# Optimization experiments

Measured on AMD Instinct MI355X. Metric: run time of the kernel, lower is better.

Reference implementation:

```python
import jax, jax.numpy as jnp
import numpy as np

K = 3
PAD = 1


def bilinear_gather(xr, py, px):
    # xr: [B, G, H, W, C] channels-last per offset group; py/px: [B, G, H, W] sample coords
    B, G, H, W, C = xr.shape
    y0 = jnp.floor(py)
    x0 = jnp.floor(px)
    wy = py - y0
    wx = px - x0
    y0i = y0.astype(jnp.int32)
    x0i = x0.astype(jnp.int32)
    bi = jnp.arange(B)[:, None, None, None]
    gi = jnp.arange(G)[None, :, None, None]
    out = jnp.zeros(py.shape + (C,), xr.dtype)
    corners = (
        (0, 0, (1 - wy) * (1 - wx)),
        (0, 1, (1 - wy) * wx),
        (1, 0, wy * (1 - wx)),
        (1, 1, wy * wx),
    )
    for dy_, dx_, w in corners:
        yy = y0i + dy_
        xx = x0i + dx_
        valid = ((yy >= 0) & (yy < H) & (xx >= 0) & (xx < W)).astype(xr.dtype)
        yc = jnp.clip(yy, 0, H - 1)
        xc = jnp.clip(xx, 0, W - 1)
        v = xr[bi, gi, yc, xc]  # [B,G,H,W,C]
        out = out + (w * valid)[..., None] * v
    return out


def setup_inputs() -> dict:
    key = jax.random.key(0)
    k1, k2, k3, k4, k5 = jax.random.split(key, 5)
    B, Cin, H, W = 4, 64, 256, 256
    G, OC = 8, 64
    KK = K * K
    x = jax.random.normal(k1, (B, Cin, H, W), jnp.float32)
    offset = jax.random.normal(k2, (B, 2, G * KK, H, W), jnp.float32)
    mask = jax.random.normal(k3, (B, G * KK, H, W), jnp.float32)
    weight = jax.random.normal(k4, (OC, Cin // G, K, K), jnp.float32) * 0.05
    bias = jax.random.normal(k5, (OC,), jnp.float32) * 0.01
    return {"x": x, "offset": offset, "mask": mask, "weight": weight, "bias": bias}


def reference(x, offset, mask, weight, bias):
    B, Cin, H, W = x.shape
    OC, Cpg, _, _ = weight.shape
    G = Cin // Cpg          # conv groups == offset groups here
    OPG = OC // G
    KK = K * K
    # replicate module's permute(0,2,1,3,4).flip(1).view(b,-1,fh,fw):
    # pair axis (dy,dx) is input dim 1; combined (group,tap) axis is reversed
    off = jnp.flip(offset, axis=2)                      # [B,2,G*KK,H,W]
    dy = off[:, 0].reshape(B, G, KK, H, W)
    dx = off[:, 1].reshape(B, G, KK, H, W)
    m = jax.nn.sigmoid(mask).reshape(B, G, KK, H, W)
    xr = x.reshape(B, G, Cpg, H, W).transpose(0, 1, 3, 4, 2)  # [B,G,H,W,Cpg]
    wg = weight.reshape(G, OPG, Cpg, K, K)
    iy = jnp.arange(H, dtype=x.dtype)[None, None, :, None]
    ix = jnp.arange(W, dtype=x.dtype)[None, None, None, :]
    out = jnp.zeros((B, G, OPG, H, W), x.dtype)
    for t in range(KK):  # fixed small loop over kernel taps
        ki, kj = t // K, t % K
        py = iy - PAD + ki + dy[:, :, t]
        px = ix - PAD + kj + dx[:, :, t]
        s = bilinear_gather(xr, py, px) * m[:, :, t][..., None]  # [B,G,H,W,Cpg]
        out = out + jnp.einsum('bghwc,gdc->bgdhw', s, wg[:, :, :, ki, kj])
    return out.reshape(B, OC, H, W) + bias[None, :, None, None]
```

## Files before the change

### kernel.cpp

```cpp
#include <hip/hip_runtime.h>
#include <hip/hip_fp16.h>


#define KSZ 3
#define PAD 1

static constexpr int B   = 4;
static constexpr int Cin = 64;
static constexpr int H   = 256;
static constexpr int W   = 256;
static constexpr int G   = 8;
static constexpr int OC  = 64;
static constexpr int KK  = KSZ * KSZ;
static constexpr int Cpg = Cin / G;
static constexpr int OPG = OC / G;
static constexpr int HW  = H * W;
static constexpr int NXCD = 8;

static constexpr int BR    = 4;
static constexpr int BC    = 64;
static constexpr int MARG  = 5;
static constexpr int WROWS = BR + 2 * MARG + 1;
static constexpr int WCOLS = 75;
static constexpr int WUSED = BC + 2 * MARG;

typedef _Float16 f16x8  __attribute__((ext_vector_type(8)));
typedef float    f32x16 __attribute__((ext_vector_type(16)));

union U4H {
    uint4 u;
    __half2 h2[4];
    _Float16 h[8];
    f16x8 v;
};

__global__ __launch_bounds__(256) void transpose_kernel(
    const float* __restrict__ x, uint4* __restrict__ xt)
{
    const int h = blockIdx.x, g = blockIdx.y, b = blockIdx.z;
    const int w = threadIdx.x;
    const int pix = h * W + w;
    const float* src = x + (size_t)(b * Cin + g * Cpg) * HW + pix;
    U4H v;
#pragma unroll
    for (int c = 0; c < 8; ++c) v.h[c] = (_Float16)src[(size_t)c * HW];
    xt[(size_t)(b * G + g) * HW + pix] = v.u;
}

__global__ __launch_bounds__(320) void prep_weights(
    const float* __restrict__ weight, uint4* __restrict__ wfrag)
{
    const int g    = blockIdx.x;
    const int tid  = threadIdx.x;
    const int m    = tid >> 6;
    const int lane = tid & 63;
    const int hi   = lane >> 5;
    const int lp   = lane & 31;
    const int t    = 2 * m + hi;
    U4H a;
#pragma unroll
    for (int c = 0; c < 8; ++c) {
        float v = 0.0f;
        if (lp < OPG && t < KK)
            v = weight[((size_t)(g * OPG + lp) * Cpg + c) * KK + t];
        a.h[c] = (_Float16)v;
    }
    wfrag[((size_t)g * 5 + m) * 64 + lane] = a.u;
}

__global__ __launch_bounds__(256) void dcn_kernel(
    const uint4* __restrict__ xt,
    const uint4* __restrict__ wfrag,
    const float* __restrict__ offset,
    const float* __restrict__ mask,
    const float* __restrict__ bias,
    float* __restrict__ out)
{
    __shared__ uint4 win[WROWS * WCOLS];

    const unsigned id = blockIdx.x;
    const unsigned wl = (id & (NXCD - 1)) * (gridDim.x / NXCD) + (id >> 3);
    const int colblk = wl & 3;
    const int rowblk = (wl >> 2) & 63;
    const int g      = (wl >> 8) & (G - 1);
    const int b      = wl >> 11;

    const int h_base = rowblk * BR;
    const int xbase  = colblk * BC;
    const int h0     = h_base - MARG;
    const int x0base = xbase - MARG;

    const int tid  = threadIdx.x;
    const int lane = tid & 63;
    const int wave = tid >> 6;
    const int hi   = lane >> 5;
    const int lp   = lane & 31;

    const int h = h_base + wave;

    const uint4* xb = xt + (size_t)(b * G + g) * HW;

#pragma unroll
    for (int it = 0; it < 5; ++it) {
        const int k = it * 256 + tid;
        if (k < WROWS * WCOLS) {
            const int i = k / WCOLS;
            const int j = k - i * WCOLS;
            const int gr = min(max(h0 + i, 0), H - 1);
            const int gc = min(max(x0base + j, 0), W - 1);
            win[k] = xb[gr * W + gc];
        }
    }

    f16x8 afrag[5];
    {
        const uint4* wf = wfrag + (size_t)g * 5 * 64 + lane;
#pragma unroll
        for (int m = 0; m < 5; ++m) {
            U4H tmp; tmp.u = wf[m * 64];
            afrag[m] = tmp.v;
        }
    }

    const float* offy = offset + (size_t)(b * 2 + 0) * (G * KK) * HW;
    const float* offx = offset + (size_t)(b * 2 + 1) * (G * KK) * HW;
    const float* mk   = mask + (size_t)b * (G * KK) * HW;

    float dyv[2][5], dxv[2][5], msv[2][5];
#pragma unroll
    for (int tile = 0; tile < 2; ++tile) {
        const int wq  = xbase + tile * 32 + lp;
        const int pix = h * W + wq;
#pragma unroll
        for (int m = 0; m < 5; ++m) {
            const int t  = 2 * m + hi;
            const int tt = (t > 8) ? 8 : t;
            const int idx0 = G * KK - 1 - (g * KK + tt);
            dyv[tile][m] = offy[(size_t)idx0 * HW + pix];
            dxv[tile][m] = offx[(size_t)idx0 * HW + pix];
            const float mv = mk[(size_t)(g * KK + tt) * HW + pix];
            float s = 1.0f / (1.0f + __expf(-mv));
            msv[tile][m] = (t <= 8) ? s : 0.0f;
        }
    }

    __syncthreads();

    auto sample = [&](int t, int wq, float dy, float dx, float msig) -> f16x8 {
        const int tt = (t > 8) ? 8 : t;
        const int ki = (tt >= 3) + (tt >= 6);
        const int kj = tt - 3 * ki;

        const float py = (float)(h - PAD + ki) + dy;
        const float px = (float)(wq - PAD + kj) + dx;
        const float y0f = floorf(py), x0f = floorf(px);
        const float wy = py - y0f, wx = px - x0f;
        const int y0 = (int)y0f, x0 = (int)x0f;
        const int iy0 = y0 - h0;
        const int ix0 = x0 - x0base;

        float w00, w01, w10, w11;
        uint4 v00, v01, v10, v11;

        const bool ok = (y0 >= 0) & (y0 + 1 < H) & (x0 >= 0) & (x0 + 1 < W) &
                        ((unsigned)iy0 <= (unsigned)(WROWS - 2)) &
                        ((unsigned)ix0 <= (unsigned)(WUSED - 2));
        if (__all((int)ok)) {
            const float u = (1.f - wy) * msig, v = wy * msig;
            w00 = u * (1.f - wx); w01 = u * wx;
            w10 = v * (1.f - wx); w11 = v * wx;
            const int a0 = iy0 * WCOLS + ix0;
            v00 = win[a0];         v01 = win[a0 + 1];
            v10 = win[a0 + WCOLS]; v11 = win[a0 + WCOLS + 1];
        } else {
            const bool vy0 = (y0 >= 0) & (y0 < H), vy1 = (y0 + 1 >= 0) & (y0 + 1 < H);
            const bool vx0 = (x0 >= 0) & (x0 < W), vx1 = (x0 + 1 >= 0) & (x0 + 1 < W);
            const float u   = vy0 ? (1.f - wy) * msig : 0.f;
            const float v   = vy1 ? wy * msig : 0.f;
            const float cx0 = vx0 ? (1.f - wx) : 0.f;
            const float cx1 = vx1 ? wx : 0.f;
            w00 = u * cx0; w01 = u * cx1; w10 = v * cx0; w11 = v * cx1;

            const int i0  = min(max(iy0, 0), WROWS - 1);
            const int i1  = min(max(iy0 + 1, 0), WROWS - 1);
            const int jx0 = min(max(ix0, 0), WUSED - 1);
            const int jx1 = min(max(ix0 + 1, 0), WUSED - 1);
            v00 = win[i0 * WCOLS + jx0];
            v01 = win[i0 * WCOLS + jx1];
            v10 = win[i1 * WCOLS + jx0];
            v11 = win[i1 * WCOLS + jx1];

            const bool bad =
                (vy0 & ((unsigned)iy0 > (unsigned)(WROWS - 1))) |
                (vy1 & ((unsigned)(iy0 + 1) > (unsigned)(WROWS - 1))) |
                (vx0 & ((unsigned)ix0 > (unsigned)(WUSED - 1))) |
                (vx1 & ((unsigned)(ix0 + 1) > (unsigned)(WUSED - 1)));
            if (__builtin_expect(__any((int)bad), 0)) {
                if (bad) {
                    const int yc0 = min(max(y0, 0), H - 1);
                    const int yc1 = min(max(y0 + 1, 0), H - 1);
                    const int xc0 = min(max(x0, 0), W - 1);
                    const int xc1 = min(max(x0 + 1, 0), W - 1);
                    v00 = xb[yc0 * W + xc0];
                    v01 = xb[yc0 * W + xc1];
                    v10 = xb[yc1 * W + xc0];
                    v11 = xb[yc1 * W + xc1];
                }
            }
        }

        U4H a, bq, c, d; a.u = v00; bq.u = v01; c.u = v10; d.u = v11;
        const __half2 hw00 = __float2half2_rn(w00);
        const __half2 hw01 = __float2half2_rn(w01);
        const __half2 hw10 = __float2half2_rn(w10);
        const __half2 hw11 = __float2half2_rn(w11);
        U4H s;
#pragma unroll
        for (int i = 0; i < 4; ++i)
            s.h2[i] = __hfma2(hw00, a.h2[i],
                      __hfma2(hw01, bq.h2[i],
                      __hfma2(hw10, c.h2[i],
                      __hmul2(hw11, d.h2[i]))));
        return s.v;
    };

    f32x16 acc0 = {};
    f32x16 acc1 = {};
    {
        const int wq = xbase + lp;
#pragma unroll
        for (int m = 0; m < 5; ++m)
            acc0 = __builtin_amdgcn_mfma_f32_32x32x16_f16(
                afrag[m], sample(2 * m + hi, wq, dyv[0][m], dxv[0][m], msv[0][m]), acc0, 0, 0, 0);
    }
    {
        const int wq = xbase + 32 + lp;
#pragma unroll
        for (int m = 0; m < 5; ++m)
            acc1 = __builtin_amdgcn_mfma_f32_32x32x16_f16(
                afrag[m], sample(2 * m + hi, wq, dyv[1][m], dxv[1][m], msv[1][m]), acc1, 0, 0, 0);
    }

#pragma unroll
    for (int tile = 0; tile < 2; ++tile) {
        const int wq = xbase + tile * 32 + lp;
#pragma unroll
        for (int r = 0; r < 4; ++r) {
            const int dd = r + 4 * hi;
            const float v = (tile == 0 ? acc0[r] : acc1[r]) + bias[g * OPG + dd];
            out[((size_t)b * OC + g * OPG + dd) * HW + h * W + wq] = v;
        }
    }
}

extern "C" void kernel_launch(void* const* d_in, const int* in_sizes, int n_in,
                              void* d_out, int out_size, void* d_ws, size_t ws_size,
                              hipStream_t stream) {
    const float* x      = (const float*)d_in[0];
    const float* offset = (const float*)d_in[1];
    const float* mask   = (const float*)d_in[2];
    const float* weight = (const float*)d_in[3];
    const float* bias   = (const float*)d_in[4];
    float* out = (float*)d_out;

    uint4* xt    = (uint4*)d_ws;
    uint4* wfrag = (uint4*)((char*)d_ws + (size_t)B * G * HW * 16);

    dim3 tgrid(H, G, B);
    transpose_kernel<<<tgrid, dim3(256), 0, stream>>>(x, xt);
    prep_weights<<<dim3(G), dim3(320), 0, stream>>>(weight, wfrag);
    dcn_kernel<<<dim3(B * G * (H / BR) * (W / BC)), dim3(256), 0, stream>>>(
        xt, wfrag, offset, mask, bias, out);
}
```

Baseline: 98.19 us.

## Zero-pad LDS window and interleave sample issue with MFMA across two tiles

The shared-memory window now stores zeros for out-of-image pixels, so the fast path only checks window bounds and drops the image-boundary tests. Sampling is split into an issue step, which computes coordinates and launches the four LDS reads, and a finish step, which blends them. The two 32-column tiles are interleaved per tap so LDS latency overlaps with MFMA work. The fallback path to global memory stays for lanes outside the window, and holding two tiles' corner data at once raises register pressure.

```diff
diff --git a/kernel.cpp b/kernel.cpp
--- a/kernel.cpp
+++ b/kernel.cpp
@@ -34,6 +34,13 @@
     f16x8 v;
 };
 
+struct Pend {
+    float wy, wx, ms;
+    int   iy0, ix0;
+    bool  ok;
+    uint4 c00, c01, c10, c11;
+};
+
 __global__ __launch_bounds__(256) void transpose_kernel(
     const float* __restrict__ x, uint4* __restrict__ xt)
 {
@@ -106,9 +113,14 @@
         if (k < WROWS * WCOLS) {
             const int i = k / WCOLS;
             const int j = k - i * WCOLS;
-            const int gr = min(max(h0 + i, 0), H - 1);
-            const int gc = min(max(x0base + j, 0), W - 1);
-            win[k] = xb[gr * W + gc];
+            const int gr = h0 + i;
+            const int gc = x0base + j;
+            const bool vld = ((unsigned)gr < (unsigned)H) & ((unsigned)gc < (unsigned)W);
+            const int grc = min(max(gr, 0), H - 1);
+            const int gcc = min(max(gc, 0), W - 1);
+            uint4 val = xb[grc * W + gcc];
+            if (!vld) val = make_uint4(0, 0, 0, 0);
+            win[k] = val;
         }
     }
 
@@ -144,101 +156,81 @@
         }
     }
 
-    __syncthreads();
-
-    auto sample = [&](int t, int wq, float dy, float dx, float msig) -> f16x8 {
+    float pyb[5], pxb0[5], pxb1[5];
+#pragma unroll
+    for (int m = 0; m < 5; ++m) {
+        const int t  = 2 * m + hi;
         const int tt = (t > 8) ? 8 : t;
         const int ki = (tt >= 3) + (tt >= 6);
         const int kj = tt - 3 * ki;
-
-        const float py = (float)(h - PAD + ki) + dy;
-        const float px = (float)(wq - PAD + kj) + dx;
+        pyb[m]  = (float)(h - PAD + ki);
+        pxb0[m] = (float)(xbase + lp - PAD + kj);
+        pxb1[m] = pxb0[m] + 32.0f;
+    }
+
+    __syncthreads();
+
+    auto issue = [&](float pybm, float pxbm, float dy, float dx, float ms) -> Pend {
+        Pend p;
+        const float py = pybm + dy;
+        const float px = pxbm + dx;
         const float y0f = floorf(py), x0f = floorf(px);
-        const float wy = py - y0f, wx = px - x0f;
-        const int y0 = (int)y0f, x0 = (int)x0f;
-        const int iy0 = y0 - h0;
-        const int ix0 = x0 - x0base;
-
-        float w00, w01, w10, w11;
-        uint4 v00, v01, v10, v11;
-
-        const bool ok = (y0 >= 0) & (y0 + 1 < H) & (x0 >= 0) & (x0 + 1 < W) &
-                        ((unsigned)iy0 <= (unsigned)(WROWS - 2)) &
-                        ((unsigned)ix0 <= (unsigned)(WUSED - 2));
-        if (__all((int)ok)) {
-            const float u = (1.f - wy) * msig, v = wy * msig;
-            w00 = u * (1.f - wx); w01 = u * wx;
-            w10 = v * (1.f - wx); w11 = v * wx;
-            const int a0 = iy0 * WCOLS + ix0;
-            v00 = win[a0];         v01 = win[a0 + 1];
-            v10 = win[a0 + WCOLS]; v11 = win[a0 + WCOLS + 1];
-        } else {
-            const bool vy0 = (y0 >= 0) & (y0 < H), vy1 = (y0 + 1 >= 0) & (y0 + 1 < H);
-            const bool vx0 = (x0 >= 0) & (x0 < W), vx1 = (x0 + 1 >= 0) & (x0 + 1 < W);
-            const float u   = vy0 ? (1.f - wy) * msig : 0.f;
-            const float v   = vy1 ? wy * msig : 0.f;
-            const float cx0 = vx0 ? (1.f - wx) : 0.f;
-            const float cx1 = vx1 ? wx : 0.f;
-            w00 = u * cx0; w01 = u * cx1; w10 = v * cx0; w11 = v * cx1;
-
-            const int i0  = min(max(iy0, 0), WROWS - 1);
-            const int i1  = min(max(iy0 + 1, 0), WROWS - 1);
-            const int jx0 = min(max(ix0, 0), WUSED - 1);
-            const int jx1 = min(max(ix0 + 1, 0), WUSED - 1);
-            v00 = win[i0 * WCOLS + jx0];
-            v01 = win[i0 * WCOLS + jx1];
-            v10 = win[i1 * WCOLS + jx0];
-            v11 = win[i1 * WCOLS + jx1];
-
-            const bool bad =
-                (vy0 & ((unsigned)iy0 > (unsigned)(WROWS - 1))) |
-                (vy1 & ((unsigned)(iy0 + 1) > (unsigned)(WROWS - 1))) |
-                (vx0 & ((unsigned)ix0 > (unsigned)(WUSED - 1))) |
-                (vx1 & ((unsigned)(ix0 + 1) > (unsigned)(WUSED - 1)));
-            if (__builtin_expect(__any((int)bad), 0)) {
-                if (bad) {
-                    const int yc0 = min(max(y0, 0), H - 1);
-                    const int yc1 = min(max(y0 + 1, 0), H - 1);
-                    const int xc0 = min(max(x0, 0), W - 1);
-                    const int xc1 = min(max(x0 + 1, 0), W - 1);
-                    v00 = xb[yc0 * W + xc0];
-                    v01 = xb[yc0 * W + xc1];
-                    v10 = xb[yc1 * W + xc0];
-                    v11 = xb[yc1 * W + xc1];
-                }
+        p.wy = py - y0f;
+        p.wx = px - x0f;
+        p.ms = ms;
+        p.iy0 = (int)y0f - h0;
+        p.ix0 = (int)x0f - x0base;
+        p.ok = ((unsigned)p.iy0 <= (unsigned)(WROWS - 2)) &
+               ((unsigned)p.ix0 <= (unsigned)(WUSED - 2));
+        int a0 = p.iy0 * WCOLS + p.ix0;
+        a0 = p.ok ? a0 : 0;
+        p.c00 = win[a0];         p.c01 = win[a0 + 1];
+        p.c10 = win[a0 + WCOLS]; p.c11 = win[a0 + WCOLS + 1];
+        return p;
+    };
+
+    auto finish = [&](Pend p) -> f16x8 {
+        const float u  = (1.f - p.wy) * p.ms;
+        const float vv = p.wy * p.ms;
+        const float cx0 = 1.f - p.wx, cx1 = p.wx;
+        float w00 = u * cx0, w01 = u * cx1, w10 = vv * cx0, w11 = vv * cx1;
+        if (__builtin_expect(!__all((int)p.ok), 0)) {
+            if (!p.ok) {
+                const int y0 = p.iy0 + h0, x0 = p.ix0 + x0base;
+                const bool vy0 = (y0 >= 0) & (y0 < H), vy1 = (y0 + 1 >= 0) & (y0 + 1 < H);
+                const bool vx0 = (x0 >= 0) & (x0 < W), vx1 = (x0 + 1 >= 0) & (x0 + 1 < W);
+                const float uu = vy0 ? u : 0.f,  vz = vy1 ? vv : 0.f;
+                const float ca = vx0 ? cx0 : 0.f, cb = vx1 ? cx1 : 0.f;
+                w00 = uu * ca; w01 = uu * cb; w10 = vz * ca; w11 = vz * cb;
+                const int yc0 = min(max(y0, 0), H - 1), yc1 = min(max(y0 + 1, 0), H - 1);
+                const int xc0 = min(max(x0, 0), W - 1), xc1 = min(max(x0 + 1, 0), W - 1);
+                p.c00 = xb[yc0 * W + xc0]; p.c01 = xb[yc0 * W + xc1];
+                p.c10 = xb[yc1 * W + xc0]; p.c11 = xb[yc1 * W + xc1];
             }
         }
-
-        U4H a, bq, c, d; a.u = v00; bq.u = v01; c.u = v10; d.u = v11;
-        const __half2 hw00 = __float2half2_rn(w00);
-        const __half2 hw01 = __float2half2_rn(w01);
-        const __half2 hw10 = __float2half2_rn(w10);
-        const __half2 hw11 = __float2half2_rn(w11);
+        U4H a, bq, c, d; a.u = p.c00; bq.u = p.c01; c.u = p.c10; d.u = p.c11;
+        const __half2 h00 = __float2half2_rn(w00);
+        const __half2 h01 = __float2half2_rn(w01);
+        const __half2 h10 = __float2half2_rn(w10);
+        const __half2 h11 = __float2half2_rn(w11);
         U4H s;
 #pragma unroll
         for (int i = 0; i < 4; ++i)
-            s.h2[i] = __hfma2(hw00, a.h2[i],
-                      __hfma2(hw01, bq.h2[i],
-                      __hfma2(hw10, c.h2[i],
-                      __hmul2(hw11, d.h2[i]))));
+            s.h2[i] = __hfma2(h00, a.h2[i],
+                      __hfma2(h01, bq.h2[i],
+                      __hfma2(h10, c.h2[i],
+                      __hmul2(h11, d.h2[i]))));
         return s.v;
     };
 
     f32x16 acc0 = {};
     f32x16 acc1 = {};
-    {
-        const int wq = xbase + lp;
-#pragma unroll
-        for (int m = 0; m < 5; ++m)
-            acc0 = __builtin_amdgcn_mfma_f32_32x32x16_f16(
-                afrag[m], sample(2 * m + hi, wq, dyv[0][m], dxv[0][m], msv[0][m]), acc0, 0, 0, 0);
-    }
-    {
-        const int wq = xbase + 32 + lp;
-#pragma unroll
-        for (int m = 0; m < 5; ++m)
-            acc1 = __builtin_amdgcn_mfma_f32_32x32x16_f16(
-                afrag[m], sample(2 * m + hi, wq, dyv[1][m], dxv[1][m], msv[1][m]), acc1, 0, 0, 0);
+#pragma unroll
+    for (int m = 0; m < 5; ++m) {
+        Pend p0 = issue(pyb[m], pxb0[m], dyv[0][m], dxv[0][m], msv[0][m]);
+        Pend p1 = issue(pyb[m], pxb1[m], dyv[1][m], dxv[1][m], msv[1][m]);
+        acc0 = __builtin_amdgcn_mfma_f32_32x32x16_f16(afrag[m], finish(p0), acc0, 0, 0, 0);
+        acc1 = __builtin_amdgcn_mfma_f32_32x32x16_f16(afrag[m], finish(p1), acc1, 0, 0, 0);
     }
 
 #pragma unroll
```

Result: slower. 106.2 us (+8.2%).
